# Performance work log

Measured on AMD Instinct MI355X. Metric: run time of the kernel, lower is better.

The kernel has to match this reference:

```python
import jax, jax.numpy as jnp
import numpy as np

EPS = 1e-5
N_LANG = 5

def _ln(x, gamma, beta):
    mu = jnp.mean(x, axis=-1, keepdims=True)
    var = jnp.mean((x - mu) ** 2, axis=-1, keepdims=True)
    return (x - mu) * jax.lax.rsqrt(var + EPS) * gamma + beta

def setup_inputs() -> dict:
    key = jax.random.key(0)
    ks = jax.random.split(key, 20)
    B, S, E, T, H = 16, 512, 768, 768, 1024
    s = lambda fan_in: 1.0 / np.sqrt(fan_in)
    inp = {
        'ner_features': jax.random.normal(ks[0], (B, S, E), jnp.float32),
        'topic_features': jax.random.normal(ks[1], (B, S, T), jnp.float32),
        'language_ids': jax.random.randint(ks[2], (B,), 0, N_LANG, jnp.int64),
        # ner transform: Linear(E,H) + LayerNorm(H)
        'W_ner': jax.random.uniform(ks[3], (E, H), jnp.float32, -s(E), s(E)),
        'b_ner': jnp.zeros((H,), jnp.float32),
        'g_ner': jnp.ones((H,), jnp.float32),
        'be_ner': jnp.zeros((H,), jnp.float32),
        # topic transform: Linear(T,H) + LayerNorm(H)
        'W_top': jax.random.uniform(ks[4], (T, H), jnp.float32, -s(T), s(T)),
        'b_top': jnp.zeros((H,), jnp.float32),
        'g_top': jnp.ones((H,), jnp.float32),
        'be_top': jnp.zeros((H,), jnp.float32),
        # 5 language gate networks, stacked on leading lang axis
        'Wg1': jax.random.uniform(ks[5], (N_LANG, 2 * H, H), jnp.float32, -s(2 * H), s(2 * H)),
        'bg1': jnp.zeros((N_LANG, H), jnp.float32),
        'gg': jnp.ones((N_LANG, H), jnp.float32),
        'bg': jnp.zeros((N_LANG, H), jnp.float32),
        'Wg2': jax.random.uniform(ks[6], (N_LANG, H, 2), jnp.float32, -s(H), s(H)),
        'bg2': jnp.zeros((N_LANG, 2), jnp.float32),
    }
    return inp

def reference(ner_features, topic_features, language_ids,
              W_ner, b_ner, g_ner, be_ner,
              W_top, b_top, g_top, be_top,
              Wg1, bg1, gg, bg, Wg2, bg2):
    # shared transforms: [B,S,H]
    ner_t = jax.nn.relu(_ln(ner_features @ W_ner + b_ner, g_ner, be_ner))
    top_t = jax.nn.relu(_ln(topic_features @ W_top + b_top, g_top, be_top))
    combined = jnp.concatenate([ner_t, top_t], axis=-1)  # [B,S,2H]
    # all-language gate MLPs (faithful to the original redundant compute)
    h = jnp.einsum('bsd,ldh->lbsh', combined, Wg1) + bg1[:, None, None, :]
    h = jax.nn.relu(_ln(h, gg[:, None, None, :], bg[:, None, None, :]))
    gates_all = jax.nn.sigmoid(jnp.einsum('lbsh,lhk->lbsk', h, Wg2) + bg2[:, None, None, :])  # [L,B,S,2]
    mask = (language_ids[None, :] == jnp.arange(N_LANG)[:, None]).astype(gates_all.dtype)  # [L,B]
    gates = jnp.einsum('lb,lbsk->bsk', mask, gates_all)  # [B,S,2]
    gated_ner = ner_t * gates[..., 0:1]
    gated_topic = top_t * gates[..., 1:2]
    # dropout in eval mode (identity) for determinism
    return gated_ner, gated_topic
```

## Files before the change

### kernel.cpp

```cpp
#include <hip/hip_runtime.h>

typedef __attribute__((ext_vector_type(8))) short short8;
typedef __attribute__((ext_vector_type(4))) float f32x4;

__device__ __forceinline__ float bf2f(unsigned short u) {
    union { unsigned int i; float f; } v; v.i = ((unsigned int)u) << 16; return v.f;
}
__device__ __forceinline__ unsigned short f2bf(float f) {
    union { float f; unsigned int i; } v; v.f = f;
    unsigned int r = v.i + 0x7fffu + ((v.i >> 16) & 1u);
    return (unsigned short)(r >> 16);
}
__device__ __forceinline__ void gload16(const unsigned short* g, unsigned short* l) {
    __builtin_amdgcn_global_load_lds(
        (const __attribute__((address_space(1))) unsigned int*)g,
        (__attribute__((address_space(3))) unsigned int*)l, 16, 0, 0);
}

template<int K, int MODE>
__global__ __launch_bounds__(512, 2) void gemm8(
    const unsigned short* __restrict__ A,
    const unsigned short* __restrict__ Bta,
    const unsigned short* __restrict__ Btb,
    const float* __restrict__ biasa,
    const float* __restrict__ biasb,
    unsigned short* __restrict__ Cb,
    const int* __restrict__ lang)
{
    constexpr int BN  = (MODE == 0) ? 256 : 128;
    constexpr int MR  = (MODE == 0) ? 8 : 4;
    constexpr int MPC = MR / 4;
    constexpr int NBLK = 1024 / BN;
    constexpr int LPT = 4 + BN / 64;
    constexpr int NT  = K / 64;

    __shared__ __align__(16) unsigned short As[2][256][64];
    __shared__ __align__(16) unsigned short Bs[2][BN][64];

    const int t = threadIdx.x;
    const int nwg = gridDim.x;
    const int bid = blockIdx.x;
    const int swz = (bid & 7) * (nwg >> 3) + (bid >> 3);
    const int mb = swz / NBLK;
    const int nb = swz % NBLK;
    const int gm0 = mb * 256, gn0 = nb * BN;

    const unsigned short* Bt;
    const float* bias;
    int sel = 0;
    if (MODE == 0) {
        sel = gm0 >> 13;
        Bt = sel ? Btb : Bta;
        bias = sel ? biasb : biasa;
    } else {
        const int l = lang[gm0 >> 9];
        Bt = Bta + (size_t)l * ((size_t)K * 1024);
        bias = biasa + l * 1024;
    }

    const int lane = t & 63, w = t >> 6;
    const int wm = (MODE == 0) ? (w >> 2) : (w >> 1);
    const int wn = (MODE == 0) ? (w & 3) : (w & 1);
    const int fr = lane & 15, g4 = lane >> 4, f7 = lane & 7;

    const int sr  = t >> 3;
    const int gsw = ((t & 7) ^ (sr & 7)) * 8;
    const int lc  = (t & 7) * 8;
    const unsigned short* ag = A  + (size_t)(gm0 + sr) * K + gsw;
    const unsigned short* bg = Bt + (size_t)(gn0 + sr) * K + gsw;

    f32x4 acc[MR][4];
#pragma unroll
    for (int m = 0; m < MR; ++m)
#pragma unroll
        for (int n = 0; n < 4; ++n)
            acc[m][n] = (f32x4){0.f, 0.f, 0.f, 0.f};

    auto stage = [&](int buf, int k0) {
#pragma unroll
        for (int i = 0; i < 4; ++i)
            gload16(ag + (size_t)(i * 64) * K + k0, &As[buf][i * 64 + sr][lc]);
#pragma unroll
        for (int i = 0; i < BN / 64; ++i)
            gload16(bg + (size_t)(i * 64) * K + k0, &Bs[buf][i * 64 + sr][lc]);
    };

    stage(0, 0);
    if (NT > 1) stage(1, 64);

    for (int tt = 0; tt < NT; ++tt) {
        const int cur = tt & 1;
        if (tt + 1 < NT) asm volatile("s_waitcnt vmcnt(%0)" :: "i"(LPT) : "memory");
        else             asm volatile("s_waitcnt vmcnt(0)" ::: "memory");
        __builtin_amdgcn_s_barrier();
        asm volatile("" ::: "memory");
        __builtin_amdgcn_sched_barrier(0);

        short8 bf_[4][2];
#pragma unroll
        for (int n = 0; n < 4; ++n)
#pragma unroll
            for (int kk = 0; kk < 2; ++kk)
                bf_[n][kk] = *(const short8*)&Bs[cur][wn * 64 + n * 16 + fr][((kk * 4 + g4) ^ f7) * 8];

#pragma unroll
        for (int c = 0; c < 4; ++c) {
            short8 af_[MPC][2];
#pragma unroll
            for (int mm = 0; mm < MPC; ++mm)
#pragma unroll
                for (int kk = 0; kk < 2; ++kk)
                    af_[mm][kk] = *(const short8*)&As[cur][wm * (MR * 16) + (c * MPC + mm) * 16 + fr][((kk * 4 + g4) ^ f7) * 8];
            __builtin_amdgcn_s_setprio(1);
#pragma unroll
            for (int mm = 0; mm < MPC; ++mm)
#pragma unroll
                for (int n = 0; n < 4; ++n)
#pragma unroll
                    for (int kk = 0; kk < 2; ++kk)
                        acc[c * MPC + mm][n] = __builtin_amdgcn_mfma_f32_16x16x32_bf16(
                            af_[mm][kk], bf_[n][kk], acc[c * MPC + mm][n], 0, 0, 0);
            __builtin_amdgcn_s_setprio(0);
        }

        __builtin_amdgcn_sched_barrier(0);
        __builtin_amdgcn_s_barrier();
        asm volatile("" ::: "memory");
        if (tt + 2 < NT) stage(cur, (tt + 2) * 64);
    }

    const int fq = lane >> 4;
    const size_t pitch  = (MODE == 0) ? 2048 : 1024;
    const size_t coloff = (MODE == 0) ? (size_t)sel * 1024 : 0;
    const int rbase = (MODE == 0) ? (gm0 & 8191) : gm0;
#pragma unroll
    for (int n = 0; n < 4; ++n) {
        const int col = gn0 + wn * 64 + n * 16 + fr;
        const float bv = bias[col];
#pragma unroll
        for (int m = 0; m < MR; ++m) {
            const int row0 = rbase + wm * (MR * 16) + m * 16 + fq * 4;
#pragma unroll
            for (int r = 0; r < 4; ++r)
                Cb[(size_t)(row0 + r) * pitch + coloff + col] = f2bf(acc[m][n][r] + bv);
        }
    }
}

__global__ __launch_bounds__(256) void wt_bf16(
    const float* __restrict__ W, unsigned short* __restrict__ Wt, int K, int N)
{
    __shared__ float tile[32][33];
    W  += (size_t)blockIdx.z * K * N;
    Wt += (size_t)blockIdx.z * K * N;
    const int n0 = blockIdx.x * 32, k0 = blockIdx.y * 32;
    const int x = threadIdx.x & 31, y = threadIdx.x >> 5;
#pragma unroll
    for (int i = 0; i < 4; ++i)
        tile[y + 8 * i][x] = W[(size_t)(k0 + y + 8 * i) * N + n0 + x];
    __syncthreads();
#pragma unroll
    for (int i = 0; i < 4; ++i)
        Wt[(size_t)(n0 + y + 8 * i) * K + k0 + x] = f2bf(tile[x][y + 8 * i]);
}

__global__ __launch_bounds__(256) void conv_bf16(
    const float* __restrict__ in, unsigned short* __restrict__ out)
{
    const size_t i = ((size_t)blockIdx.x * 256 + threadIdx.x) * 8;
    const float4 a = ((const float4*)(in + i))[0];
    const float4 b = ((const float4*)(in + i))[1];
    ushort4 u, v;
    u.x = f2bf(a.x); u.y = f2bf(a.y); u.z = f2bf(a.z); u.w = f2bf(a.w);
    v.x = f2bf(b.x); v.y = f2bf(b.y); v.z = f2bf(b.z); v.w = f2bf(b.w);
    *(ushort4*)(out + i)     = u;
    *(ushort4*)(out + i + 4) = v;
}

__global__ __launch_bounds__(256) void ln_relu_c(
    unsigned short* __restrict__ comb,
    const float* __restrict__ gn, const float* __restrict__ bn,
    const float* __restrict__ gt, const float* __restrict__ btp)
{
    const int b = blockIdx.x, t = threadIdx.x;
    const int r = b >> 1, half = b & 1;
    unsigned short* p = comb + (size_t)r * 2048 + half * 1024 + t * 4;
    ushort4 u = *(const ushort4*)p;
    const float x0 = bf2f(u.x), x1 = bf2f(u.y), x2 = bf2f(u.z), x3 = bf2f(u.w);
    float s1 = x0 + x1 + x2 + x3;
    float s2 = x0 * x0 + x1 * x1 + x2 * x2 + x3 * x3;
#pragma unroll
    for (int off = 32; off > 0; off >>= 1) {
        s1 += __shfl_down(s1, off);
        s2 += __shfl_down(s2, off);
    }
    __shared__ float red[8];
    const int wid = t >> 6;
    if ((t & 63) == 0) { red[wid] = s1; red[4 + wid] = s2; }
    __syncthreads();
    s1 = red[0] + red[1] + red[2] + red[3];
    s2 = red[4] + red[5] + red[6] + red[7];
    const float mean = s1 * (1.0f / 1024.0f);
    const float var = fmaxf(s2 * (1.0f / 1024.0f) - mean * mean, 0.0f);
    const float rstd = rsqrtf(var + 1e-5f);
    const float* G  = half ? gt : gn;
    const float* Be = half ? btp : bn;
    const float4 g  = ((const float4*)G)[t];
    const float4 be = ((const float4*)Be)[t];
    u.x = f2bf(fmaxf((x0 - mean) * rstd * g.x + be.x, 0.0f));
    u.y = f2bf(fmaxf((x1 - mean) * rstd * g.y + be.y, 0.0f));
    u.z = f2bf(fmaxf((x2 - mean) * rstd * g.z + be.z, 0.0f));
    u.w = f2bf(fmaxf((x3 - mean) * rstd * g.w + be.w, 0.0f));
    *(ushort4*)p = u;
}

__global__ __launch_bounds__(256) void ln_gate(
    const unsigned short* __restrict__ preln, const unsigned short* __restrict__ comb,
    const float* __restrict__ gg, const float* __restrict__ bgb,
    const float* __restrict__ Wg2, const float* __restrict__ bg2,
    const int* __restrict__ lang,
    float* __restrict__ outN, float* __restrict__ outT)
{
    const int r = blockIdx.x, t = threadIdx.x;
    const int l = lang[r >> 9];
    const ushort4 u = *(const ushort4*)(preln + (size_t)r * 1024 + t * 4);
    const float x0 = bf2f(u.x), x1 = bf2f(u.y), x2 = bf2f(u.z), x3 = bf2f(u.w);
    float s1 = x0 + x1 + x2 + x3;
    float s2 = x0 * x0 + x1 * x1 + x2 * x2 + x3 * x3;
#pragma unroll
    for (int off = 32; off > 0; off >>= 1) {
        s1 += __shfl_down(s1, off);
        s2 += __shfl_down(s2, off);
    }
    __shared__ float red[8];
    const int wid = t >> 6;
    if ((t & 63) == 0) { red[wid] = s1; red[4 + wid] = s2; }
    __syncthreads();
    s1 = red[0] + red[1] + red[2] + red[3];
    s2 = red[4] + red[5] + red[6] + red[7];
    const float mean = s1 * (1.0f / 1024.0f);
    const float var = fmaxf(s2 * (1.0f / 1024.0f) - mean * mean, 0.0f);
    const float rstd = rsqrtf(var + 1e-5f);
    const float4 g  = ((const float4*)(gg + l * 1024))[t];
    const float4 be = ((const float4*)(bgb + l * 1024))[t];
    const float h0 = fmaxf((x0 - mean) * rstd * g.x + be.x, 0.0f);
    const float h1 = fmaxf((x1 - mean) * rstd * g.y + be.y, 0.0f);
    const float h2 = fmaxf((x2 - mean) * rstd * g.z + be.z, 0.0f);
    const float h3 = fmaxf((x3 - mean) * rstd * g.w + be.w, 0.0f);
    const float4* W = (const float4*)(Wg2 + (size_t)l * 2048);
    const float4 wa = W[t * 2], wb = W[t * 2 + 1];
    float d0 = h0 * wa.x + h1 * wa.z + h2 * wb.x + h3 * wb.z;
    float d1 = h0 * wa.y + h1 * wa.w + h2 * wb.y + h3 * wb.w;
#pragma unroll
    for (int off = 32; off > 0; off >>= 1) {
        d0 += __shfl_down(d0, off);
        d1 += __shfl_down(d1, off);
    }
    __syncthreads();
    if ((t & 63) == 0) { red[wid] = d0; red[4 + wid] = d1; }
    __syncthreads();
    d0 = red[0] + red[1] + red[2] + red[3] + bg2[l * 2 + 0];
    d1 = red[4] + red[5] + red[6] + red[7] + bg2[l * 2 + 1];
    const float g0 = 1.0f / (1.0f + __expf(-d0));
    const float g1 = 1.0f / (1.0f + __expf(-d1));
    const ushort4 cn = *(const ushort4*)(comb + (size_t)r * 2048 + t * 4);
    const ushort4 ct = *(const ushort4*)(comb + (size_t)r * 2048 + 1024 + t * 4);
    float4 a, b;
    a.x = bf2f(cn.x) * g0; a.y = bf2f(cn.y) * g0; a.z = bf2f(cn.z) * g0; a.w = bf2f(cn.w) * g0;
    b.x = bf2f(ct.x) * g1; b.y = bf2f(ct.y) * g1; b.z = bf2f(ct.z) * g1; b.w = bf2f(ct.w) * g1;
    ((float4*)(outN + (size_t)r * 1024))[t] = a;
    ((float4*)(outT + (size_t)r * 1024))[t] = b;
}

extern "C" void kernel_launch(void* const* d_in, const int* in_sizes, int n_in,
                              void* d_out, int out_size, void* d_ws, size_t ws_size,
                              hipStream_t stream)
{
    const float* ner    = (const float*)d_in[0];
    const float* top    = (const float*)d_in[1];
    const int*   lang   = (const int*)d_in[2];
    const float* W_ner  = (const float*)d_in[3];
    const float* b_ner  = (const float*)d_in[4];
    const float* g_ner  = (const float*)d_in[5];
    const float* be_ner = (const float*)d_in[6];
    const float* W_top  = (const float*)d_in[7];
    const float* b_top  = (const float*)d_in[8];
    const float* g_top  = (const float*)d_in[9];
    const float* be_top = (const float*)d_in[10];
    const float* Wg1    = (const float*)d_in[11];
    const float* bg1    = (const float*)d_in[12];
    const float* gg     = (const float*)d_in[13];
    const float* bgb    = (const float*)d_in[14];
    const float* Wg2    = (const float*)d_in[15];
    const float* bg2    = (const float*)d_in[16];

    float* out  = (float*)d_out;
    float* outN = out;
    float* outT = out + 8388608;

    char* ws = (char*)d_ws;
    unsigned short* combined = (unsigned short*)ws;
    unsigned short* actb     = (unsigned short*)(ws + 33554432);
    unsigned short* preln2   = (unsigned short*)(ws + 33554432);
    unsigned short* Wg1t     = (unsigned short*)(ws + 58720256);
    unsigned short* W_nert   = (unsigned short*)outT;
    unsigned short* W_topt   = W_nert + 786432;

    wt_bf16<<<dim3(32, 24, 1), 256, 0, stream>>>(W_ner, W_nert, 768, 1024);
    wt_bf16<<<dim3(32, 24, 1), 256, 0, stream>>>(W_top, W_topt, 768, 1024);
    wt_bf16<<<dim3(32, 64, 5), 256, 0, stream>>>(Wg1, Wg1t, 2048, 1024);

    conv_bf16<<<3072, 256, 0, stream>>>(ner, actb);
    conv_bf16<<<3072, 256, 0, stream>>>(top, actb + 6291456);

    gemm8<768, 0><<<256, 512, 0, stream>>>(
        actb, W_nert, W_topt, b_ner, b_top, combined, nullptr);
    ln_relu_c<<<16384, 256, 0, stream>>>(combined, g_ner, be_ner, g_top, be_top);

    gemm8<2048, 1><<<256, 512, 0, stream>>>(
        combined, Wg1t, nullptr, bg1, nullptr, preln2, lang);

    ln_gate<<<8192, 256, 0, stream>>>(preln2, combined, gg, bgb, Wg2, bg2, lang, outN, outT);
}
```

Measured before the change: 152.3 us.

## Use 128x128 tiles, split-K gate GEMM into fp32 partials, fuse prep kernels

Replaces the 256-row, 512-thread GEMM with a 128x128-tile, 256-thread kernel that uses K-steps of 32, giving a grid of 1024 workgroups. The gate GEMM is split into two K halves that write fp32 partial sums into the two output buffers, and ln_gate adds them before the LayerNorm. The five weight-transpose and conversion launches are merged into one prep kernel. This targets better occupancy, load balance and launch overhead, at the cost of less data reuse per tile and more fp32 traffic for the partials.

```diff
diff --git a/kernel.cpp b/kernel.cpp
--- a/kernel.cpp
+++ b/kernel.cpp
@@ -17,144 +17,142 @@
         (__attribute__((address_space(3))) unsigned int*)l, 16, 0, 0);
 }
 
-template<int K, int MODE>
-__global__ __launch_bounds__(512, 2) void gemm8(
+template<int KPITCH, int KLEN, int MODE>
+__global__ __launch_bounds__(256, 4) void gemm_ks(
     const unsigned short* __restrict__ A,
     const unsigned short* __restrict__ Bta,
     const unsigned short* __restrict__ Btb,
     const float* __restrict__ biasa,
     const float* __restrict__ biasb,
-    unsigned short* __restrict__ Cb,
+    void* __restrict__ Cbv,
     const int* __restrict__ lang)
 {
-    constexpr int BN  = (MODE == 0) ? 256 : 128;
-    constexpr int MR  = (MODE == 0) ? 8 : 4;
-    constexpr int MPC = MR / 4;
-    constexpr int NBLK = 1024 / BN;
-    constexpr int LPT = 4 + BN / 64;
-    constexpr int NT  = K / 64;
-
-    __shared__ __align__(16) unsigned short As[2][256][64];
-    __shared__ __align__(16) unsigned short Bs[2][BN][64];
+    constexpr int NT = KLEN / 32;
+    __shared__ __align__(16) unsigned short As[2][128][32];
+    __shared__ __align__(16) unsigned short Bs[2][128][32];
 
     const int t = threadIdx.x;
     const int nwg = gridDim.x;
     const int bid = blockIdx.x;
     const int swz = (bid & 7) * (nwg >> 3) + (bid >> 3);
-    const int mb = swz / NBLK;
-    const int nb = swz % NBLK;
-    const int gm0 = mb * 256, gn0 = nb * BN;
-
+
+    int gm0, gn0, koff = 0, sel = 0;
     const unsigned short* Bt;
     const float* bias;
-    int sel = 0;
     if (MODE == 0) {
+        gm0 = (swz >> 3) * 128;
+        gn0 = (swz & 7) * 128;
         sel = gm0 >> 13;
         Bt = sel ? Btb : Bta;
         bias = sel ? biasb : biasa;
     } else {
+        const int ks = swz & 1, rem = swz >> 1;
+        gm0 = (rem >> 3) * 128;
+        gn0 = (rem & 7) * 128;
+        koff = ks * KLEN;
         const int l = lang[gm0 >> 9];
-        Bt = Bta + (size_t)l * ((size_t)K * 1024);
-        bias = biasa + l * 1024;
+        Bt = Bta + (size_t)l * ((size_t)KPITCH * 1024);
+        bias = ks ? nullptr : (biasa + l * 1024);
     }
 
     const int lane = t & 63, w = t >> 6;
-    const int wm = (MODE == 0) ? (w >> 2) : (w >> 1);
-    const int wn = (MODE == 0) ? (w & 3) : (w & 1);
-    const int fr = lane & 15, g4 = lane >> 4, f7 = lane & 7;
-
-    const int sr  = t >> 3;
-    const int gsw = ((t & 7) ^ (sr & 7)) * 8;
-    const int lc  = (t & 7) * 8;
-    const unsigned short* ag = A  + (size_t)(gm0 + sr) * K + gsw;
-    const unsigned short* bg = Bt + (size_t)(gn0 + sr) * K + gsw;
-
-    f32x4 acc[MR][4];
-#pragma unroll
-    for (int m = 0; m < MR; ++m)
+    const int wm = w >> 1, wn = w & 1;
+    const int fr = lane & 15, g4 = lane >> 4;
+    const int fkey = (fr & 3) ^ ((fr >> 2) & 3);
+    const int csw = (g4 ^ fkey) * 8;
+
+    const int sr   = t >> 2;
+    const int slot = t & 3;
+    const int key  = (sr & 3) ^ ((sr >> 2) & 3);
+    const int gc   = (slot ^ key) * 8;
+    const unsigned short* ag = A  + (size_t)(gm0 + sr) * KPITCH + koff + gc;
+    const unsigned short* bg = Bt + (size_t)(gn0 + sr) * KPITCH + koff + gc;
+
+    f32x4 acc[4][4];
+#pragma unroll
+    for (int m = 0; m < 4; ++m)
 #pragma unroll
         for (int n = 0; n < 4; ++n)
             acc[m][n] = (f32x4){0.f, 0.f, 0.f, 0.f};
 
-    auto stage = [&](int buf, int k0) {
-#pragma unroll
-        for (int i = 0; i < 4; ++i)
-            gload16(ag + (size_t)(i * 64) * K + k0, &As[buf][i * 64 + sr][lc]);
-#pragma unroll
-        for (int i = 0; i < BN / 64; ++i)
-            gload16(bg + (size_t)(i * 64) * K + k0, &Bs[buf][i * 64 + sr][lc]);
+    auto stage = [&](int buf, int kb) {
+#pragma unroll
+        for (int i = 0; i < 2; ++i)
+            gload16(ag + (size_t)(i * 64) * KPITCH + kb, &As[buf][i * 64 + sr][slot * 8]);
+#pragma unroll
+        for (int i = 0; i < 2; ++i)
+            gload16(bg + (size_t)(i * 64) * KPITCH + kb, &Bs[buf][i * 64 + sr][slot * 8]);
     };
+    auto compute = [&](int c) {
+        short8 af[4], bf[4];
+#pragma unroll
+        for (int m = 0; m < 4; ++m) af[m] = *(const short8*)&As[c][wm * 64 + m * 16 + fr][csw];
+#pragma unroll
+        for (int n = 0; n < 4; ++n) bf[n] = *(const short8*)&Bs[c][wn * 64 + n * 16 + fr][csw];
+        __builtin_amdgcn_s_setprio(1);
+#pragma unroll
+        for (int m = 0; m < 4; ++m)
+#pragma unroll
+            for (int n = 0; n < 4; ++n)
+                acc[m][n] = __builtin_amdgcn_mfma_f32_16x16x32_bf16(af[m], bf[n], acc[m][n], 0, 0, 0);
+        __builtin_amdgcn_s_setprio(0);
+    };
 
     stage(0, 0);
-    if (NT > 1) stage(1, 64);
-
-    for (int tt = 0; tt < NT; ++tt) {
-        const int cur = tt & 1;
-        if (tt + 1 < NT) asm volatile("s_waitcnt vmcnt(%0)" :: "i"(LPT) : "memory");
-        else             asm volatile("s_waitcnt vmcnt(0)" ::: "memory");
+    stage(1, 32);
+    for (int u = 0; u < NT; ++u) {
+        if (u + 1 < NT) asm volatile("s_waitcnt vmcnt(4)" ::: "memory");
+        else            asm volatile("s_waitcnt vmcnt(0)" ::: "memory");
         __builtin_amdgcn_s_barrier();
         asm volatile("" ::: "memory");
         __builtin_amdgcn_sched_barrier(0);
-
-        short8 bf_[4][2];
-#pragma unroll
-        for (int n = 0; n < 4; ++n)
-#pragma unroll
-            for (int kk = 0; kk < 2; ++kk)
-                bf_[n][kk] = *(const short8*)&Bs[cur][wn * 64 + n * 16 + fr][((kk * 4 + g4) ^ f7) * 8];
-
-#pragma unroll
-        for (int c = 0; c < 4; ++c) {
-            short8 af_[MPC][2];
-#pragma unroll
-            for (int mm = 0; mm < MPC; ++mm)
-#pragma unroll
-                for (int kk = 0; kk < 2; ++kk)
-                    af_[mm][kk] = *(const short8*)&As[cur][wm * (MR * 16) + (c * MPC + mm) * 16 + fr][((kk * 4 + g4) ^ f7) * 8];
-            __builtin_amdgcn_s_setprio(1);
-#pragma unroll
-            for (int mm = 0; mm < MPC; ++mm)
-#pragma unroll
-                for (int n = 0; n < 4; ++n)
-#pragma unroll
-                    for (int kk = 0; kk < 2; ++kk)
-                        acc[c * MPC + mm][n] = __builtin_amdgcn_mfma_f32_16x16x32_bf16(
-                            af_[mm][kk], bf_[n][kk], acc[c * MPC + mm][n], 0, 0, 0);
-            __builtin_amdgcn_s_setprio(0);
-        }
-
+        compute(u & 1);
         __builtin_amdgcn_sched_barrier(0);
         __builtin_amdgcn_s_barrier();
         asm volatile("" ::: "memory");
-        if (tt + 2 < NT) stage(cur, (tt + 2) * 64);
+        if (u + 2 < NT) stage(u & 1, (u + 2) * 32);
     }
 
     const int fq = lane >> 4;
-    const size_t pitch  = (MODE == 0) ? 2048 : 1024;
-    const size_t coloff = (MODE == 0) ? (size_t)sel * 1024 : 0;
-    const int rbase = (MODE == 0) ? (gm0 & 8191) : gm0;
-#pragma unroll
-    for (int n = 0; n < 4; ++n) {
-        const int col = gn0 + wn * 64 + n * 16 + fr;
-        const float bv = bias[col];
-#pragma unroll
-        for (int m = 0; m < MR; ++m) {
-            const int row0 = rbase + wm * (MR * 16) + m * 16 + fq * 4;
-#pragma unroll
-            for (int r = 0; r < 4; ++r)
-                Cb[(size_t)(row0 + r) * pitch + coloff + col] = f2bf(acc[m][n][r] + bv);
+    if (MODE == 0) {
+        unsigned short* Cb = (unsigned short*)Cbv;
+        const int rbase = gm0 & 8191;
+        const size_t coloff = (size_t)sel * 1024;
+#pragma unroll
+        for (int n = 0; n < 4; ++n) {
+            const int col = gn0 + wn * 64 + n * 16 + fr;
+            const float bv = bias[col];
+#pragma unroll
+            for (int m = 0; m < 4; ++m) {
+                const int row0 = rbase + wm * 64 + m * 16 + fq * 4;
+#pragma unroll
+                for (int r = 0; r < 4; ++r)
+                    Cb[(size_t)(row0 + r) * 2048 + coloff + col] = f2bf(acc[m][n][r] + bv);
+            }
         }
-    }
-}
-
-__global__ __launch_bounds__(256) void wt_bf16(
-    const float* __restrict__ W, unsigned short* __restrict__ Wt, int K, int N)
-{
-    __shared__ float tile[32][33];
-    W  += (size_t)blockIdx.z * K * N;
-    Wt += (size_t)blockIdx.z * K * N;
-    const int n0 = blockIdx.x * 32, k0 = blockIdx.y * 32;
-    const int x = threadIdx.x & 31, y = threadIdx.x >> 5;
+    } else {
+        float* C = (float*)Cbv + (koff ? 8388608u : 0u);
+#pragma unroll
+        for (int n = 0; n < 4; ++n) {
+            const int col = gn0 + wn * 64 + n * 16 + fr;
+            const float bv = bias ? bias[col] : 0.0f;
+#pragma unroll
+            for (int m = 0; m < 4; ++m) {
+                const int row0 = gm0 + wm * 64 + m * 16 + fq * 4;
+#pragma unroll
+                for (int r = 0; r < 4; ++r)
+                    C[(size_t)(row0 + r) * 1024 + col] = acc[m][n][r] + bv;
+            }
+        }
+    }
+}
+
+__device__ __forceinline__ void wt_tile(
+    const float* W, unsigned short* Wt, int K, int N, int bx, int by,
+    float (*tile)[33], int t)
+{
+    const int n0 = bx * 32, k0 = by * 32;
+    const int x = t & 31, y = t >> 5;
 #pragma unroll
     for (int i = 0; i < 4; ++i)
         tile[y + 8 * i][x] = W[(size_t)(k0 + y + 8 * i) * N + n0 + x];
@@ -163,18 +161,43 @@
     for (int i = 0; i < 4; ++i)
         Wt[(size_t)(n0 + y + 8 * i) * K + k0 + x] = f2bf(tile[x][y + 8 * i]);
 }
-
-__global__ __launch_bounds__(256) void conv_bf16(
-    const float* __restrict__ in, unsigned short* __restrict__ out)
-{
-    const size_t i = ((size_t)blockIdx.x * 256 + threadIdx.x) * 8;
+__device__ __forceinline__ void conv_chunk(
+    const float* in, unsigned short* out, int b, int t)
+{
+    const size_t i = ((size_t)b * 256 + t) * 8;
     const float4 a = ((const float4*)(in + i))[0];
-    const float4 b = ((const float4*)(in + i))[1];
+    const float4 c = ((const float4*)(in + i))[1];
     ushort4 u, v;
     u.x = f2bf(a.x); u.y = f2bf(a.y); u.z = f2bf(a.z); u.w = f2bf(a.w);
-    v.x = f2bf(b.x); v.y = f2bf(b.y); v.z = f2bf(b.z); v.w = f2bf(b.w);
+    v.x = f2bf(c.x); v.y = f2bf(c.y); v.z = f2bf(c.z); v.w = f2bf(c.w);
     *(ushort4*)(out + i)     = u;
     *(ushort4*)(out + i + 4) = v;
+}
+
+__global__ __launch_bounds__(256) void prep_all(
+    const float* __restrict__ W_ner, unsigned short* __restrict__ W_nert,
+    const float* __restrict__ W_top, unsigned short* __restrict__ W_topt,
+    const float* __restrict__ Wg1,   unsigned short* __restrict__ Wg1t,
+    const float* __restrict__ ner,   const float* __restrict__ top,
+    unsigned short* __restrict__ actb)
+{
+    __shared__ float tile[32][33];
+    int b = blockIdx.x;
+    const int t = threadIdx.x;
+    if (b < 768)  { wt_tile(W_ner, W_nert, 768, 1024, b % 32, b / 32, tile, t); return; }
+    b -= 768;
+    if (b < 768)  { wt_tile(W_top, W_topt, 768, 1024, b % 32, b / 32, tile, t); return; }
+    b -= 768;
+    if (b < 10240) {
+        const int z = b / 2048, r = b % 2048;
+        wt_tile(Wg1 + (size_t)z * 2097152, Wg1t + (size_t)z * 2097152,
+                2048, 1024, r % 32, r / 32, tile, t);
+        return;
+    }
+    b -= 10240;
+    if (b < 3072) { conv_chunk(ner, actb, b, t); return; }
+    b -= 3072;
+    conv_chunk(top, actb + 6291456, b, t);
 }
 
 __global__ __launch_bounds__(256) void ln_relu_c(
@@ -215,16 +238,17 @@
 }
 
 __global__ __launch_bounds__(256) void ln_gate(
-    const unsigned short* __restrict__ preln, const unsigned short* __restrict__ comb,
-    const float* __restrict__ gg, const float* __restrict__ bgb,
-    const float* __restrict__ Wg2, const float* __restrict__ bg2,
-    const int* __restrict__ lang,
-    float* __restrict__ outN, float* __restrict__ outT)
+    const float* pa, const float* pb, const unsigned short* comb,
+    const float* gg, const float* bgb,
+    const float* Wg2, const float* bg2, const int* lang,
+    float* outN, float* outT)
 {
     const int r = blockIdx.x, t = threadIdx.x;
     const int l = lang[r >> 9];
-    const ushort4 u = *(const ushort4*)(preln + (size_t)r * 1024 + t * 4);
-    const float x0 = bf2f(u.x), x1 = bf2f(u.y), x2 = bf2f(u.z), x3 = bf2f(u.w);
+    const float4 va = ((const float4*)(pa + (size_t)r * 1024))[t];
+    const float4 vb = ((const float4*)(pb + (size_t)r * 1024))[t];
+    const float x0 = va.x + vb.x, x1 = va.y + vb.y;
+    const float x2 = va.z + vb.z, x3 = va.w + vb.w;
     float s1 = x0 + x1 + x2 + x3;
     float s2 = x0 * x0 + x1 * x1 + x2 * x2 + x3 * x3;
 #pragma unroll
@@ -301,24 +325,20 @@
     char* ws = (char*)d_ws;
     unsigned short* combined = (unsigned short*)ws;
     unsigned short* actb     = (unsigned short*)(ws + 33554432);
-    unsigned short* preln2   = (unsigned short*)(ws + 33554432);
     unsigned short* Wg1t     = (unsigned short*)(ws + 58720256);
     unsigned short* W_nert   = (unsigned short*)outT;
     unsigned short* W_topt   = W_nert + 786432;
 
-    wt_bf16<<<dim3(32, 24, 1), 256, 0, stream>>>(W_ner, W_nert, 768, 1024);
-    wt_bf16<<<dim3(32, 24, 1), 256, 0, stream>>>(W_top, W_topt, 768, 1024);
-    wt_bf16<<<dim3(32, 64, 5), 256, 0, stream>>>(Wg1, Wg1t, 2048, 1024);
-
-    conv_bf16<<<3072, 256, 0, stream>>>(ner, actb);
-    conv_bf16<<<3072, 256, 0, stream>>>(top, actb + 6291456);
-
-    gemm8<768, 0><<<256, 512, 0, stream>>>(
+    prep_all<<<17920, 256, 0, stream>>>(W_ner, W_nert, W_top, W_topt,
+                                        Wg1, Wg1t, ner, top, actb);
+
+    gemm_ks<768, 768, 0><<<1024, 256, 0, stream>>>(
         actb, W_nert, W_topt, b_ner, b_top, combined, nullptr);
     ln_relu_c<<<16384, 256, 0, stream>>>(combined, g_ner, be_ner, g_top, be_top);
 
-    gemm8<2048, 1><<<256, 512, 0, stream>>>(
-        combined, Wg1t, nullptr, bg1, nullptr, preln2, lang);
-
-    ln_gate<<<8192, 256, 0, stream>>>(preln2, combined, gg, bgb, Wg2, bg2, lang, outN, outT);
-}
+    gemm_ks<2048, 1024, 1><<<1024, 256, 0, stream>>>(
+        combined, Wg1t, nullptr, bg1, nullptr, out, lang);
+
+    ln_gate<<<8192, 256, 0, stream>>>(outN, outT, combined, gg, bgb, Wg2, bg2,
+                                      lang, outN, outT);
+}
```

New measurement: 152.8 us. Within noise of the previous version (+0.3%).
